# Optimization experiments

Hardware: AMD Instinct MI355X
Metric: run time of the kernel (lower is better)

## Reference

```python
import jax, jax.numpy as jnp
import numpy as np
from jax import lax

BLOCK = 64      # block_size
OVERLAP = 16
NITER = 64      # Niter init kwarg; loop runs min(1000, Niter)
L = 0.24        # diffusion step size
K = 0.03        # exp(logk), logk = log(0.03)
DEPS = 0.1
FFT_STEPS = 10
THRESH = 0.1    # uniform-region variance threshold


def _g(x):
    # g(x) = 1 / (1 + |x^2| / K^2)
    return 1.0 / (1.0 + jnp.abs(x * x) / (K * K))


def _avgpool3(x):
    # F.avg_pool2d(x, 3, stride=1, padding=1) with count_include_pad=True (divide by 9)
    s = lax.reduce_window(x, 0.0, lax.add, (1, 1, 3, 3), (1, 1, 1, 1),
                          [(0, 0), (0, 0), (1, 1), (1, 1)])
    return s / 9.0


def _fft_diffuse_block(block, bcv, bch):
    cv_mean = bcv.mean()
    ch_mean = bch.mean()
    h, w = block.shape[2], block.shape[3]
    ky = jnp.arange(h, dtype=block.dtype)[:, None] * (2.0 * np.pi / h)      # [h,1]
    kx = jnp.arange(w // 2 + 1, dtype=block.dtype)[None, :] * (2.0 * np.pi / w)  # [1,w//2+1]
    op = (1.0 - 2.0 * L * (cv_mean * (1.0 - jnp.cos(ky)) + ch_mean * (1.0 - jnp.cos(kx)))) ** FFT_STEPS
    return jnp.fft.irfft2(jnp.fft.rfft2(block) * op, s=(h, w))


def _forward(guide, initial):
    # depth shift for stability (torch code branches on initial.min() <= deps)
    shift = jnp.where(initial.min() <= DEPS, DEPS, 0.0).astype(initial.dtype)
    depth = initial + shift

    # diffusion coefficients from guide: cv [B,1,H-1,W], ch [B,1,H,W-1]
    cv = _g(jnp.mean(jnp.abs(guide[:, :, 1:, :] - guide[:, :, :-1, :]), axis=1, keepdims=True))
    ch = _g(jnp.mean(jnp.abs(guide[:, :, :, 1:] - guide[:, :, :, :-1]), axis=1, keepdims=True))

    # identify_uniform_regions (local variance via avg pools); original torch code
    # broadcasts shapes (H-1,W) & (H,W-1) which errors -- we crop to common (H-1,W-1)
    cv_var = _avgpool3(cv ** 2) - _avgpool3(cv) ** 2
    ch_var = _avgpool3(ch ** 2) - _avgpool3(ch) ** 2
    uniform = ((cv_var[:, :, :, :-1] < THRESH) & (ch_var[:, :, :-1, :] < THRESH)).astype(depth.dtype)

    B, C, H, W = depth.shape
    step = BLOCK - OVERLAP
    # sequential per-block FFT diffusion with overlap blending (blocks read
    # depth updated by previous blocks, so order matters)
    for b in range(B):
        for y in range(0, H, step):
            for x in range(0, W, step):
                y_end = min(y + BLOCK, H)
                x_end = min(x + BLOCK, W)
                bh, bw = y_end - y, x_end - x
                block = depth[b:b + 1, :, y:y_end, x:x_end]
                bcv = cv[b:b + 1, :, y:y_end - 1, x:x_end]
                bch = ch[b:b + 1, :, y:y_end, x:x_end - 1]
                bun = uniform[b:b + 1, :, y:y_end, x:x_end]  # clips at edges (H-1,W-1)
                cond = bun.mean() > 0.7
                newb = _fft_diffuse_block(block, bcv, bch)
                if y > 0 or x > 0:
                    blend_y = jnp.ones((bh,), depth.dtype)
                    if y > 0:
                        r = jnp.arange(bh)
                        blend_y = jnp.where(r < min(OVERLAP, bh), r.astype(depth.dtype) / OVERLAP, blend_y)
                    blend_x = jnp.ones((bw,), depth.dtype)
                    if x > 0:
                        r = jnp.arange(bw)
                        blend_x = jnp.where(r < min(OVERLAP, bw), r.astype(depth.dtype) / OVERLAP, blend_x)
                    blend = (blend_y[:, None] * blend_x[None, :])[None, None]
                    cand = block * (1.0 - blend) + newb * blend
                else:
                    cand = newb
                region = jnp.where(cond, cand, block)
                depth = depth.at[b:b + 1, :, y:y_end, x:x_end].set(region)

    # explicit anisotropic diffusion stencil, serial data dependence -> lax.scan
    def diffuse_step(I, _):
        dv = I[:, :, 1:, :] - I[:, :, :-1, :]
        dh = I[:, :, :, 1:] - I[:, :, :, :-1]  # computed before vertical update (as in torch)
        tv = L * cv * dv
        I = I.at[:, :, 1:, :].add(-tv).at[:, :, :-1, :].add(tv)
        th = L * ch * dh
        I = I.at[:, :, :, 1:].add(-th).at[:, :, :, :-1].add(th)
        return I, None

    depth, _ = lax.scan(diffuse_step, depth, None, length=min(1000, NITER))
    y_pred = depth - shift
    return y_pred, cv, ch


def setup_inputs() -> dict:
    key = jax.random.key(0)
    k1, k2 = jax.random.split(key)
    guide = jax.random.uniform(k1, (2, 3, 512, 512), dtype=jnp.float32)
    initial = jax.random.uniform(k2, (2, 1, 512, 512), dtype=jnp.float32)
    return {"guide": guide, "initial": initial}


def reference(guide, initial):
    # returns (y_pred, cv, ch) matching {'y_pred':..., 'cv':..., 'ch':...}
    return _forward(guide, initial)
```

## Files before the change

### kernel.cpp

```cpp
#include <hip/hip_runtime.h>
#include <stdint.h>

#define LDIFF 0.24f

constexpr int H = 512, W = 512, NB = 2;
constexpr int HW = H * W;
constexpr int N_D = NB * HW;
constexpr int CVH = 511, CVW = 512;
constexpr int CHH = 512, CHW = 511;
constexpr int N_CV = NB * CVH * CVW;
constexpr int NBLKS = 11;
constexpr int NBT = NB * 121;

__device__ inline float ldc(const float* p) {
    return __hip_atomic_load(p, __ATOMIC_RELAXED, __HIP_MEMORY_SCOPE_AGENT);
}
__device__ inline void stc(float* p, float v) {
    __hip_atomic_store(p, v, __ATOMIC_RELAXED, __HIP_MEMORY_SCOPE_AGENT);
}
__device__ inline int ldci(const int* p) {
    return __hip_atomic_load(p, __ATOMIC_RELAXED, __HIP_MEMORY_SCOPE_AGENT);
}
__device__ inline void stci(int* p, int v) {
    __hip_atomic_store(p, v, __ATOMIC_RELAXED, __HIP_MEMORY_SCOPE_AGENT);
}

__device__ inline float rot_a(float x) {
    return __int_as_float(__builtin_amdgcn_update_dpp(0, __float_as_int(x), 0x134, 0xf, 0xf, false));
}
__device__ inline float rot_b(float x) {
    return __int_as_float(__builtin_amdgcn_update_dpp(0, __float_as_int(x), 0x13c, 0xf, 0xf, false));
}
__device__ inline float sh_a(float x) {
    return __int_as_float(__builtin_amdgcn_update_dpp(0, __float_as_int(x), 0x130, 0xf, 0xf, true));
}
__device__ inline float sh_b(float x) {
    return __int_as_float(__builtin_amdgcn_update_dpp(0, __float_as_int(x), 0x138, 0xf, 0xf, true));
}

__global__ __launch_bounds__(256) void kall(
    const float* __restrict__ guide, const float* __restrict__ initial,
    float* __restrict__ cv, float* __restrict__ ch,
    float* __restrict__ D, float* __restrict__ T0, float* __restrict__ T1,
    float* __restrict__ ypred, int* __restrict__ sync_)
{
    __shared__ float cvT[73 * 74];
    __shared__ float chT[73 * 74];
    __shared__ float xT[2][4][64];
    __shared__ float xB[2][4][64];
    __shared__ float red[12];
    __shared__ float prmS[3];

    int* wflag = sync_;
    int* dflag = sync_ + 16384;

    const int blk = blockIdx.x;
    const int i = blk / NBLKS, j = blk % NBLKS;
    const int b = blockIdx.y;
    const int tid = threadIdx.x;
    const int lane = tid & 63, wv = tid >> 6;
    const int r0 = wv * 16;
    const int me = b * 121 + blk;

    const int y0 = i * 48, x0 = j * 48;
    const int y1 = min(y0 + 64, 512), x1 = min(x0 + 64, 512);
    const int bh = y1 - y0, bw = x1 - x0;
    const int yb = y0 - 8, xb = x0 - 8;
    const float kinv = 1.0f / (0.03f * 0.03f);

    const float* gb = guide + (size_t)b * 3 * HW;
    for (int p = tid; p < 73 * 73; p += 256) {
        int rr = p / 73, cc2 = p - rr * 73;
        int y = yb + rr, x = xb + cc2;
        float cvv = 0.0f, chv = 0.0f;
        if (y >= 0 && y < 512 && x >= 0 && x < 512) {
            const float* g = gb + y * W + x;
            float g0 = g[0], g1 = g[HW], g2 = g[2 * HW];
            if (y < 511) {
                float d = (fabsf(g[W] - g0) + fabsf(g[HW + W] - g1) + fabsf(g[2 * HW + W] - g2)) * (1.0f / 3.0f);
                cvv = 1.0f / (1.0f + d * d * kinv);
            }
            if (x < 511) {
                float d = (fabsf(g[1] - g0) + fabsf(g[HW + 1] - g1) + fabsf(g[2 * HW + 1] - g2)) * (1.0f / 3.0f);
                chv = 1.0f / (1.0f + d * d * kinv);
            }
        }
        cvT[rr * 74 + cc2] = cvv;
        chT[rr * 74 + cc2] = chv;
    }
    __syncthreads();

    {
        int rcv = min(y0 + 48, CVH) - y0, ccv = min(x0 + 48, CVW) - x0;
        float* cvo = cv + b * CVH * CVW;
        for (int p = tid; p < rcv * ccv; p += 256) {
            int r = p / ccv, c = p - r * ccv;
            cvo[(y0 + r) * CVW + x0 + c] = cvT[(r + 8) * 74 + c + 8];
        }
        int rch = min(y0 + 48, CHH) - y0, cch = min(x0 + 48, CHW) - x0;
        float* cho = ch + b * CHH * CHW;
        for (int p = tid; p < rch * cch; p += 256) {
            int r = p / cch, c = p - r * cch;
            cho[(y0 + r) * CHW + x0 + c] = chT[(r + 8) * 74 + c + 8];
        }
    }

    float scv = 0.f, sch = 0.f, sun = 0.f;
    {
        int n = (bh - 1) * bw;
        for (int p = tid; p < n; p += 256) { int r = p / bw, c = p - r * bw; scv += cvT[(r + 8) * 74 + c + 8]; }
    }
    {
        int cols = bw - 1, n = bh * cols;
        for (int p = tid; p < n; p += 256) { int r = p / cols, c = p - r * cols; sch += chT[(r + 8) * 74 + c + 8]; }
    }
    const int ur = min(y1, 511) - y0, uc = min(x1, 511) - x0;
    {
        int n = ur * uc;
        for (int p = tid; p < n; p += 256) {
            int r = p / uc, c = p - r * uc;
            float s1 = 0.f, s2 = 0.f, t1 = 0.f, t2 = 0.f;
            #pragma unroll
            for (int dy = 0; dy < 3; dy++)
                #pragma unroll
                for (int dx = 0; dx < 3; dx++) {
                    float v = cvT[(r + 7 + dy) * 74 + c + 7 + dx]; s1 += v; s2 += v * v;
                    float w2 = chT[(r + 7 + dy) * 74 + c + 7 + dx]; t1 += w2; t2 += w2 * w2;
                }
            float m = s1 * (1.0f / 9.0f);
            float vcv = s2 * (1.0f / 9.0f) - m * m;
            m = t1 * (1.0f / 9.0f);
            float vch = t2 * (1.0f / 9.0f) - m * m;
            if (vcv < 0.1f && vch < 0.1f) sun += 1.f;
        }
    }
    #pragma unroll
    for (int m = 1; m < 64; m <<= 1) {
        scv += __shfl_xor(scv, m);
        sch += __shfl_xor(sch, m);
        sun += __shfl_xor(sun, m);
    }
    if (lane == 0) { red[wv * 3] = scv; red[wv * 3 + 1] = sch; red[wv * 3 + 2] = sun; }
    __syncthreads();
    if (tid == 0) {
        float a0 = red[0] + red[3] + red[6] + red[9];
        float a1 = red[1] + red[4] + red[7] + red[10];
        float a2 = red[2] + red[5] + red[8] + red[11];
        prmS[0] = a0 / (float)((bh - 1) * bw);
        prmS[1] = a1 / (float)(bh * (bw - 1));
        prmS[2] = (a2 / (float)(ur * uc) > 0.7f) ? 1.0f : 0.0f;
    }
    __syncthreads();

    int prb = __builtin_amdgcn_update_dpp(0, lane, 0x134, 0xf, 0xf, false);
    const bool dirL = (prb == ((lane + 63) & 63));

    const bool cond = prmS[2] > 0.5f;
    const float a = LDIFF * prmS[0], bc = LDIFF * prmS[1];
    float* Db = D + b * HW;
    const float* ini = initial + b * HW;

    const int mh = bh - 1, mw = bw - 1;
    const int ccw = lane & mw;

    if (!cond) {
        #pragma unroll
        for (int k = 0; k < 16; k++) {
            int r = r0 + k;
            if (r < bh && (i == 0 || r >= 16) && lane < bw && (j == 0 || lane >= 16)) {
                int ad = (y0 + r) * W + x0 + lane;
                stc(&Db[ad], ini[ad]);
            }
        }
        asm volatile("s_waitcnt vmcnt(0)" ::: "memory");
        if (lane == 0) stci(&wflag[me * 64 + wv * 16], 1);
    } else {
        float u[16], orig[16];
        int addr[16]; bool fD[16];
        #pragma unroll
        for (int k = 0; k < 16; k++) {
            int rr = (r0 + k) & mh;
            addr[k] = (y0 + rr) * W + x0 + ccw;
            fD[k] = (i > 0 && rr < 16) || (j > 0 && ccw < 16);
            if (!fD[k]) orig[k] = ini[addr[k]];
        }
        if (wv == 0) {
            bool need = false;
            const int* fp = &wflag[me * 64];
            if (lane < 3) {
                if (j > 0) { need = true; fp = &wflag[(b * 121 + i * NBLKS + j - 1) * 64 + (lane + 1) * 16]; }
            } else if (lane == 3) {
                if (i > 0) { need = true; fp = &wflag[(b * 121 + (i - 1) * NBLKS + j) * 64 + 3 * 16]; }
            } else if (lane == 4) {
                if (i > 0 && j < 10) { need = true; fp = &wflag[(b * 121 + (i - 1) * NBLKS + j + 1) * 64 + 3 * 16]; }
            } else if (lane == 5) {
                if (i > 0 && j > 0) { need = true; fp = &wflag[(b * 121 + (i - 1) * NBLKS + j - 1) * 64 + 3 * 16]; }
            }
            while (true) {
                int v = need ? ldci(fp) : 1;
                if (__ballot(v == 0) == 0) break;
                __builtin_amdgcn_s_sleep(0);
            }
        }
        __syncthreads();
        #pragma unroll
        for (int k = 0; k < 16; k++) if (fD[k]) orig[k] = ldc(&Db[addr[k]]);
        #pragma unroll
        for (int k = 0; k < 16; k++) u[k] = orig[k];

        int bs = 0;
        for (int it = 0; it < 10; it++) {
            xT[bs][wv][lane] = u[0];
            xB[bs][wv][lane] = u[15];
            __syncthreads();
            float ub = xB[bs][(wv + 3) & 3][lane];
            float ut = xT[bs][(wv + 1) & 3][lane];
            float nu[16];
            #pragma unroll
            for (int k = 0; k < 16; k++) {
                float up = (k == 0) ? ub : u[k - 1];
                float dn = (k == 15) ? ut : u[k + 1];
                float hsum = rot_a(u[k]) + rot_b(u[k]);
                nu[k] = u[k] + a * (up + dn - 2.0f * u[k]) + bc * (hsum - 2.0f * u[k]);
            }
            #pragma unroll
            for (int k = 0; k < 16; k++) u[k] = nu[k];
            bs ^= 1;
        }

        #pragma unroll
        for (int k = 0; k < 16; k++) {
            int r = r0 + k;
            if (r < bh && lane < bw) {
                float byw = (y0 > 0 && r < 16) ? (float)r * (1.0f / 16.0f) : 1.0f;
                float bxw = (x0 > 0 && lane < 16) ? (float)lane * (1.0f / 16.0f) : 1.0f;
                float wgt = byw * bxw;
                stc(&Db[(y0 + r) * W + x0 + lane], orig[k] * (1.0f - wgt) + u[k] * wgt);
            }
        }
        asm volatile("s_waitcnt vmcnt(0)" ::: "memory");
        if (lane == 0) stci(&wflag[me * 64 + wv * 16], 1);
    }
    __syncthreads();

    const int cx = xb + lane;
    const int gxc = min(max(cx, 0), 511);
    float cvr[16], chr[16], chl[16];
    int gyA[16];
    #pragma unroll
    for (int k = 0; k < 16; k++) {
        int cy = yb + r0 + k;
        gyA[k] = min(max(cy, 0), 511);
        cvr[k] = cvT[(r0 + k) * 74 + lane];
        chr[k] = chT[(r0 + k) * 74 + lane];
        chl[k] = dirL ? sh_a(chr[k]) : sh_b(chr[k]);
    }
    const float cvm1 = (wv == 0) ? 0.0f : cvT[(r0 - 1) * 74 + lane];

    float* Tb0 = T0 + b * HW;
    float* Tb1 = T1 + b * HW;
    float* ypb = ypred + b * HW;
    const bool cok = (lane >= 8 && lane < 56 && xb + lane < 512);

    for (int t = 1; t <= 8; t++) {
        if (wv == 0) {
            bool need = false;
            const int* fp = &wflag[me * 64];
            int thr = 1;
            if (t == 1) {
                if (lane < 36) {
                    int nb = lane >> 2;
                    int di = nb / 3 - 1, dj = nb % 3 - 1;
                    int ni = i + di, nj = j + dj;
                    if ((di | dj) != 0 && ni >= 0 && ni < NBLKS && nj >= 0 && nj < NBLKS) {
                        need = true;
                        fp = &wflag[(b * 121 + ni * NBLKS + nj) * 64 + (lane & 3) * 16];
                    }
                }
            } else {
                thr = t - 1;
                if (lane < 9) {
                    int di = lane / 3 - 1, dj = lane % 3 - 1;
                    int ni = i + di, nj = j + dj;
                    if ((di | dj) != 0 && ni >= 0 && ni < NBLKS && nj >= 0 && nj < NBLKS) {
                        need = true;
                        fp = &dflag[(b * 121 + ni * NBLKS + nj) * 16];
                    }
                }
            }
            while (true) {
                int v = need ? ldci(fp) : 0x7fffffff;
                if (__ballot(v < thr) == 0) break;
                __builtin_amdgcn_s_sleep(8);
            }
        }
        __syncthreads();
        const float* src = (t == 1) ? Db : (((t - 1) & 1) ? Tb1 : Tb0);
        float u[16];
        #pragma unroll
        for (int k = 0; k < 16; k++) u[k] = ldc(&src[gyA[k] * W + gxc]);

        int bs = 0;
        for (int it = 0; it < 8; it++) {
            xT[bs][wv][lane] = u[0];
            xB[bs][wv][lane] = u[15];
            __syncthreads();
            float ub = (wv > 0) ? xB[bs][wv - 1][lane] : u[0];
            float ut = (wv < 3) ? xT[bs][wv + 1][lane] : u[15];
            float V[16];
            #pragma unroll
            for (int k = 0; k < 16; k++) {
                float up = (k == 0) ? ub : u[k - 1];
                float dn = (k == 15) ? ut : u[k + 1];
                float cup = (k == 0) ? cvm1 : cvr[k - 1];
                V[k] = u[k] + LDIFF * cvr[k] * (dn - u[k]) - LDIFF * cup * (u[k] - up);
            }
            #pragma unroll
            for (int k = 0; k < 16; k++) {
                float rA = rot_a(V[k]);
                float rB = rot_b(V[k]);
                float lf = dirL ? rA : rB;
                float rt = dirL ? rB : rA;
                u[k] = V[k] + LDIFF * chr[k] * (rt - V[k]) - LDIFF * chl[k] * (V[k] - lf);
            }
            bs ^= 1;
        }

        if (t < 8) {
            float* dst = (t & 1) ? Tb1 : Tb0;
            if (cok) {
                #pragma unroll
                for (int k = 0; k < 16; k++) {
                    int r = r0 + k;
                    if (r >= 8 && r < 56) {
                        int y = yb + r;
                        if (y < 512) stc(&dst[y * W + xb + lane], u[k]);
                    }
                }
            }
            asm volatile("s_waitcnt vmcnt(0)" ::: "memory");
            __syncthreads();
            if (tid == 0) stci(&dflag[me * 16], t);
        } else {
            if (cok) {
                #pragma unroll
                for (int k = 0; k < 16; k++) {
                    int r = r0 + k;
                    if (r >= 8 && r < 56) {
                        int y = yb + r;
                        if (y < 512) ypb[y * W + xb + lane] = u[k];
                    }
                }
            }
        }
    }
}

extern "C" void kernel_launch(void* const* d_in, const int* in_sizes, int n_in,
                              void* d_out, int out_size, void* d_ws, size_t ws_size,
                              hipStream_t stream) {
    const float* guide   = (const float*)d_in[0];
    const float* initial = (const float*)d_in[1];
    float* y_pred = (float*)d_out;
    float* cv = y_pred + N_D;
    float* ch = cv + N_CV;

    uint8_t* w = (uint8_t*)d_ws;
    int* sync_ = (int*)w;
    float* D  = (float*)(w + 131072);
    float* T0 = (float*)(w + 131072 + (size_t)N_D * 4);
    float* T1 = (float*)(w + 131072 + (size_t)2 * N_D * 4);

    (void)hipMemsetAsync(sync_, 0, 131072, stream);
    kall<<<dim3(121, NB), 256, 0, stream>>>(guide, initial, cv, ch, D, T0, T1, y_pred, sync_);
}
```

Baseline: 322.8 us.

## Replace wave flags with sentinel-valued data polling and per-block edge buffers

Drops the per-wave write flags. Workspace data is pre-filled with a 0xFF sentinel, and consumers spin directly on the data values until they differ from the NaN pattern. The sequential block stage now publishes its right and bottom overlap strips into a per-block edge buffer, so the next block can read them without waiting on neighbour flags, and only the interior 48x48 is written to D. This removes flag round-trips and the extra barriers, at the cost of a second large memset and polling many addresses per lane. It also relies on computed values never equalling the sentinel bit pattern.

```diff
diff --git a/kernel.cpp b/kernel.cpp
--- a/kernel.cpp
+++ b/kernel.cpp
@@ -38,11 +38,12 @@
     return __int_as_float(__builtin_amdgcn_update_dpp(0, __float_as_int(x), 0x138, 0xf, 0xf, true));
 }
 
-__global__ __launch_bounds__(256) void kall(
+__global__ __launch_bounds__(256, 1) void kall(
     const float* __restrict__ guide, const float* __restrict__ initial,
     float* __restrict__ cv, float* __restrict__ ch,
-    float* __restrict__ D, float* __restrict__ T0, float* __restrict__ T1,
-    float* __restrict__ ypred, int* __restrict__ sync_)
+    float* __restrict__ D, float* __restrict__ EDG,
+    float* __restrict__ T0, float* __restrict__ T1,
+    float* __restrict__ ypred, int* __restrict__ dflag)
 {
     __shared__ float cvT[73 * 74];
     __shared__ float chT[73 * 74];
@@ -50,9 +51,6 @@
     __shared__ float xB[2][4][64];
     __shared__ float red[12];
     __shared__ float prmS[3];
-
-    int* wflag = sync_;
-    int* dflag = sync_ + 16384;
 
     const int blk = blockIdx.x;
     const int i = blk / NBLKS, j = blk % NBLKS;
@@ -159,55 +157,46 @@
     const float a = LDIFF * prmS[0], bc = LDIFF * prmS[1];
     float* Db = D + b * HW;
     const float* ini = initial + b * HW;
+    float* RG = EDG + (size_t)me * 2048;
+    float* BG = RG + 1024;
 
     const int mh = bh - 1, mw = bw - 1;
     const int ccw = lane & mw;
 
-    if (!cond) {
-        #pragma unroll
-        for (int k = 0; k < 16; k++) {
-            int r = r0 + k;
-            if (r < bh && (i == 0 || r >= 16) && lane < bw && (j == 0 || lane >= 16)) {
-                int ad = (y0 + r) * W + x0 + lane;
-                stc(&Db[ad], ini[ad]);
-            }
-        }
-        asm volatile("s_waitcnt vmcnt(0)" ::: "memory");
-        if (lane == 0) stci(&wflag[me * 64 + wv * 16], 1);
-    } else {
-        float u[16], orig[16];
-        int addr[16]; bool fD[16];
+    float u[16], orig[16];
+    {
+        const int* sp[16];
+        uint32_t pend = 0;
         #pragma unroll
         for (int k = 0; k < 16; k++) {
             int rr = (r0 + k) & mh;
-            addr[k] = (y0 + rr) * W + x0 + ccw;
-            fD[k] = (i > 0 && rr < 16) || (j > 0 && ccw < 16);
-            if (!fD[k]) orig[k] = ini[addr[k]];
-        }
-        if (wv == 0) {
-            bool need = false;
-            const int* fp = &wflag[me * 64];
-            if (lane < 3) {
-                if (j > 0) { need = true; fp = &wflag[(b * 121 + i * NBLKS + j - 1) * 64 + (lane + 1) * 16]; }
-            } else if (lane == 3) {
-                if (i > 0) { need = true; fp = &wflag[(b * 121 + (i - 1) * NBLKS + j) * 64 + 3 * 16]; }
-            } else if (lane == 4) {
-                if (i > 0 && j < 10) { need = true; fp = &wflag[(b * 121 + (i - 1) * NBLKS + j + 1) * 64 + 3 * 16]; }
-            } else if (lane == 5) {
-                if (i > 0 && j > 0) { need = true; fp = &wflag[(b * 121 + (i - 1) * NBLKS + j - 1) * 64 + 3 * 16]; }
-            }
-            while (true) {
-                int v = need ? ldci(fp) : 1;
-                if (__ballot(v == 0) == 0) break;
-                __builtin_amdgcn_s_sleep(0);
-            }
-        }
-        __syncthreads();
-        #pragma unroll
-        for (int k = 0; k < 16; k++) if (fD[k]) orig[k] = ldc(&Db[addr[k]]);
-        #pragma unroll
-        for (int k = 0; k < 16; k++) u[k] = orig[k];
-
+            const float* p = nullptr;
+            if (j > 0 && ccw < 16)
+                p = EDG + (size_t)(me - 1) * 2048 + rr * 16 + ccw;
+            else if (i > 0 && rr < 16)
+                p = (ccw >= 48) ? (EDG + (size_t)(me - NBLKS + 1) * 2048 + 1024 + rr * 64 + (ccw - 48))
+                                : (EDG + (size_t)(me - NBLKS) * 2048 + 1024 + rr * 64 + ccw);
+            sp[k] = (const int*)p;
+            if (p) pend |= 1u << k;
+            else   orig[k] = ini[(y0 + rr) * W + x0 + ccw];
+        }
+        while (pend) {
+            int vv[16];
+            #pragma unroll
+            for (int k = 0; k < 16; k++) if (pend & (1u << k)) vv[k] = ldci(sp[k]);
+            uint32_t np = 0;
+            #pragma unroll
+            for (int k = 0; k < 16; k++) if (pend & (1u << k)) {
+                if (vv[k] != -1) orig[k] = __int_as_float(vv[k]); else np |= 1u << k;
+            }
+            pend = np;
+            if (pend) __builtin_amdgcn_s_sleep(2);
+        }
+    }
+    #pragma unroll
+    for (int k = 0; k < 16; k++) u[k] = orig[k];
+
+    if (cond) {
         int bs = 0;
         for (int it = 0; it < 10; it++) {
             xT[bs][wv][lane] = u[0];
@@ -227,19 +216,27 @@
             for (int k = 0; k < 16; k++) u[k] = nu[k];
             bs ^= 1;
         }
-
-        #pragma unroll
-        for (int k = 0; k < 16; k++) {
-            int r = r0 + k;
-            if (r < bh && lane < bw) {
+    }
+
+    #pragma unroll
+    for (int k = 0; k < 16; k++) {
+        int r = r0 + k;
+        if (r < bh && lane < bw) {
+            if (cond) {
                 float byw = (y0 > 0 && r < 16) ? (float)r * (1.0f / 16.0f) : 1.0f;
                 float bxw = (x0 > 0 && lane < 16) ? (float)lane * (1.0f / 16.0f) : 1.0f;
                 float wgt = byw * bxw;
-                stc(&Db[(y0 + r) * W + x0 + lane], orig[k] * (1.0f - wgt) + u[k] * wgt);
-            }
-        }
-        asm volatile("s_waitcnt vmcnt(0)" ::: "memory");
-        if (lane == 0) stci(&wflag[me * 64 + wv * 16], 1);
+                u[k] = orig[k] * (1.0f - wgt) + u[k] * wgt;
+            }
+            if (bw == 64 && lane >= 48) stc(RG + r * 16 + (lane - 48), u[k]);
+            if (r >= 48)                stc(BG + (r - 48) * 64 + lane, u[k]);
+        }
+    }
+    #pragma unroll
+    for (int k = 0; k < 16; k++) {
+        int r = r0 + k;
+        if (r < 48 && r < bh && lane < 48 && lane < bw)
+            stc(&Db[(y0 + r) * W + x0 + lane], u[k]);
     }
     __syncthreads();
 
@@ -263,22 +260,28 @@
     const bool cok = (lane >= 8 && lane < 56 && xb + lane < 512);
 
     for (int t = 1; t <= 8; t++) {
-        if (wv == 0) {
-            bool need = false;
-            const int* fp = &wflag[me * 64];
-            int thr = 1;
-            if (t == 1) {
-                if (lane < 36) {
-                    int nb = lane >> 2;
-                    int di = nb / 3 - 1, dj = nb % 3 - 1;
-                    int ni = i + di, nj = j + dj;
-                    if ((di | dj) != 0 && ni >= 0 && ni < NBLKS && nj >= 0 && nj < NBLKS) {
-                        need = true;
-                        fp = &wflag[(b * 121 + ni * NBLKS + nj) * 64 + (lane & 3) * 16];
-                    }
-                }
-            } else {
-                thr = t - 1;
+        const float* src = (t == 1) ? Db : (((t - 1) & 1) ? Tb1 : Tb0);
+        float uc2[16];
+        if (t == 1) {
+            uint32_t pend = 0xFFFFu;
+            while (pend) {
+                int vv[16];
+                #pragma unroll
+                for (int k = 0; k < 16; k++) if (pend & (1u << k))
+                    vv[k] = ldci((const int*)(src + gyA[k] * W + gxc));
+                uint32_t np = 0;
+                #pragma unroll
+                for (int k = 0; k < 16; k++) if (pend & (1u << k)) {
+                    if (vv[k] != -1) uc2[k] = __int_as_float(vv[k]); else np |= 1u << k;
+                }
+                pend = np;
+                if (pend) __builtin_amdgcn_s_sleep(2);
+            }
+        } else {
+            if (wv == 0) {
+                bool need = false;
+                const int* fp = dflag;
+                const int thr = t - 1;
                 if (lane < 9) {
                     int di = lane / 3 - 1, dj = lane % 3 - 1;
                     int ni = i + di, nj = j + dj;
@@ -287,33 +290,31 @@
                         fp = &dflag[(b * 121 + ni * NBLKS + nj) * 16];
                     }
                 }
-            }
-            while (true) {
-                int v = need ? ldci(fp) : 0x7fffffff;
-                if (__ballot(v < thr) == 0) break;
-                __builtin_amdgcn_s_sleep(8);
-            }
-        }
-        __syncthreads();
-        const float* src = (t == 1) ? Db : (((t - 1) & 1) ? Tb1 : Tb0);
-        float u[16];
-        #pragma unroll
-        for (int k = 0; k < 16; k++) u[k] = ldc(&src[gyA[k] * W + gxc]);
+                while (true) {
+                    int v = need ? ldci(fp) : 0x7fffffff;
+                    if (__ballot(v < thr) == 0) break;
+                    __builtin_amdgcn_s_sleep(4);
+                }
+            }
+            __syncthreads();
+            #pragma unroll
+            for (int k = 0; k < 16; k++) uc2[k] = ldc(src + gyA[k] * W + gxc);
+        }
 
         int bs = 0;
         for (int it = 0; it < 8; it++) {
-            xT[bs][wv][lane] = u[0];
-            xB[bs][wv][lane] = u[15];
+            xT[bs][wv][lane] = uc2[0];
+            xB[bs][wv][lane] = uc2[15];
             __syncthreads();
-            float ub = (wv > 0) ? xB[bs][wv - 1][lane] : u[0];
-            float ut = (wv < 3) ? xT[bs][wv + 1][lane] : u[15];
+            float ub = (wv > 0) ? xB[bs][wv - 1][lane] : uc2[0];
+            float ut = (wv < 3) ? xT[bs][wv + 1][lane] : uc2[15];
             float V[16];
             #pragma unroll
             for (int k = 0; k < 16; k++) {
-                float up = (k == 0) ? ub : u[k - 1];
-                float dn = (k == 15) ? ut : u[k + 1];
+                float up = (k == 0) ? ub : uc2[k - 1];
+                float dn = (k == 15) ? ut : uc2[k + 1];
                 float cup = (k == 0) ? cvm1 : cvr[k - 1];
-                V[k] = u[k] + LDIFF * cvr[k] * (dn - u[k]) - LDIFF * cup * (u[k] - up);
+                V[k] = uc2[k] + LDIFF * cvr[k] * (dn - uc2[k]) - LDIFF * cup * (uc2[k] - up);
             }
             #pragma unroll
             for (int k = 0; k < 16; k++) {
@@ -321,7 +322,7 @@
                 float rB = rot_b(V[k]);
                 float lf = dirL ? rA : rB;
                 float rt = dirL ? rB : rA;
-                u[k] = V[k] + LDIFF * chr[k] * (rt - V[k]) - LDIFF * chl[k] * (V[k] - lf);
+                uc2[k] = V[k] + LDIFF * chr[k] * (rt - V[k]) - LDIFF * chl[k] * (V[k] - lf);
             }
             bs ^= 1;
         }
@@ -334,7 +335,7 @@
                     int r = r0 + k;
                     if (r >= 8 && r < 56) {
                         int y = yb + r;
-                        if (y < 512) stc(&dst[y * W + xb + lane], u[k]);
+                        if (y < 512) stc(&dst[y * W + xb + lane], uc2[k]);
                     }
                 }
             }
@@ -348,7 +349,7 @@
                     int r = r0 + k;
                     if (r >= 8 && r < 56) {
                         int y = yb + r;
-                        if (y < 512) ypb[y * W + xb + lane] = u[k];
+                        if (y < 512) ypb[y * W + xb + lane] = uc2[k];
                     }
                 }
             }
@@ -366,11 +367,13 @@
     float* ch = cv + N_CV;
 
     uint8_t* w = (uint8_t*)d_ws;
-    int* sync_ = (int*)w;
-    float* D  = (float*)(w + 131072);
-    float* T0 = (float*)(w + 131072 + (size_t)N_D * 4);
-    float* T1 = (float*)(w + 131072 + (size_t)2 * N_D * 4);
-
-    (void)hipMemsetAsync(sync_, 0, 131072, stream);
-    kall<<<dim3(121, NB), 256, 0, stream>>>(guide, initial, cv, ch, D, T0, T1, y_pred, sync_);
-}
+    int* dflag = (int*)w;
+    float* D   = (float*)(w + 65536);
+    float* EDG = (float*)(w + 65536 + (size_t)N_D * 4);
+    float* T0  = (float*)(w + 65536 + (size_t)N_D * 4 + (size_t)NBT * 8192);
+    float* T1  = T0 + N_D;
+
+    (void)hipMemsetAsync(w, 0, 65536, stream);
+    (void)hipMemsetAsync(w + 65536, 0xFF, (size_t)N_D * 4 + (size_t)NBT * 8192, stream);
+    kall<<<dim3(121, NB), 256, 0, stream>>>(guide, initial, cv, ch, D, EDG, T0, T1, y_pred, dflag);
+}
```

Result: slower. 360.6 us (+11.7%).

## Serialize each block-row's FFT-diffusion pass in one workgroup with LDS strip handoff

Applied to the files above, without the earlier changes.

The sequential per-block diffusion pass is now run by the j==0 workgroup of each block row, which walks the 11 blocks left to right. The right overlap strip is passed to the next block through shared memory, and the bottom strip goes to the row below through a separate global strip buffer. This replaces per-workgroup cross-block spin-waits on four quarter flags with one flag per block, plus a parameter-publish flag. The intent is to cut inter-workgroup synchronisation latency along the serial chain, at the cost of serialising each row's work onto a single workgroup while the others idle.

```diff
diff --git a/kernel.cpp b/kernel.cpp
--- a/kernel.cpp
+++ b/kernel.cpp
@@ -41,7 +41,8 @@
 __global__ __launch_bounds__(256) void kall(
     const float* __restrict__ guide, const float* __restrict__ initial,
     float* __restrict__ cv, float* __restrict__ ch,
-    float* __restrict__ D, float* __restrict__ T0, float* __restrict__ T1,
+    float* __restrict__ D, float* __restrict__ BSTR,
+    float* __restrict__ T0, float* __restrict__ T1,
     float* __restrict__ ypred, int* __restrict__ sync_)
 {
     __shared__ float cvT[73 * 74];
@@ -50,9 +51,13 @@
     __shared__ float xB[2][4][64];
     __shared__ float red[12];
     __shared__ float prmS[3];
+    __shared__ float prm2[3];
+    __shared__ float rstrip[64 * 16];
 
     int* wflag = sync_;
-    int* dflag = sync_ + 16384;
+    int* pflag = sync_ + 256;
+    int* dflag = sync_ + 1024;
+    float* PRM = (float*)(sync_ + 8192);
 
     const int blk = blockIdx.x;
     const int i = blk / NBLKS, j = blk % NBLKS;
@@ -149,99 +154,111 @@
         prmS[0] = a0 / (float)((bh - 1) * bw);
         prmS[1] = a1 / (float)(bh * (bw - 1));
         prmS[2] = (a2 / (float)(ur * uc) > 0.7f) ? 1.0f : 0.0f;
+        stc(&PRM[me * 4 + 0], prmS[0]);
+        stc(&PRM[me * 4 + 1], prmS[1]);
+        stc(&PRM[me * 4 + 2], prmS[2]);
     }
     __syncthreads();
+    asm volatile("s_waitcnt vmcnt(0)" ::: "memory");
+    if (tid == 0) stci(&pflag[me], 1);
 
     int prb = __builtin_amdgcn_update_dpp(0, lane, 0x134, 0xf, 0xf, false);
     const bool dirL = (prb == ((lane + 63) & 63));
 
-    const bool cond = prmS[2] > 0.5f;
-    const float a = LDIFF * prmS[0], bc = LDIFF * prmS[1];
     float* Db = D + b * HW;
     const float* ini = initial + b * HW;
 
-    const int mh = bh - 1, mw = bw - 1;
-    const int ccw = lane & mw;
-
-    if (!cond) {
-        #pragma unroll
-        for (int k = 0; k < 16; k++) {
-            int r = r0 + k;
-            if (r < bh && (i == 0 || r >= 16) && lane < bw && (j == 0 || lane >= 16)) {
-                int ad = (y0 + r) * W + x0 + lane;
-                stc(&Db[ad], ini[ad]);
-            }
-        }
-        asm volatile("s_waitcnt vmcnt(0)" ::: "memory");
-        if (lane == 0) stci(&wflag[me * 64 + wv * 16], 1);
-    } else {
-        float u[16], orig[16];
-        int addr[16]; bool fD[16];
-        #pragma unroll
-        for (int k = 0; k < 16; k++) {
-            int rr = (r0 + k) & mh;
-            addr[k] = (y0 + rr) * W + x0 + ccw;
-            fD[k] = (i > 0 && rr < 16) || (j > 0 && ccw < 16);
-            if (!fD[k]) orig[k] = ini[addr[k]];
-        }
-        if (wv == 0) {
-            bool need = false;
-            const int* fp = &wflag[me * 64];
-            if (lane < 3) {
-                if (j > 0) { need = true; fp = &wflag[(b * 121 + i * NBLKS + j - 1) * 64 + (lane + 1) * 16]; }
-            } else if (lane == 3) {
-                if (i > 0) { need = true; fp = &wflag[(b * 121 + (i - 1) * NBLKS + j) * 64 + 3 * 16]; }
-            } else if (lane == 4) {
-                if (i > 0 && j < 10) { need = true; fp = &wflag[(b * 121 + (i - 1) * NBLKS + j + 1) * 64 + 3 * 16]; }
-            } else if (lane == 5) {
-                if (i > 0 && j > 0) { need = true; fp = &wflag[(b * 121 + (i - 1) * NBLKS + j - 1) * 64 + 3 * 16]; }
-            }
-            while (true) {
-                int v = need ? ldci(fp) : 1;
-                if (__ballot(v == 0) == 0) break;
-                __builtin_amdgcn_s_sleep(0);
-            }
-        }
-        __syncthreads();
-        #pragma unroll
-        for (int k = 0; k < 16; k++) if (fD[k]) orig[k] = ldc(&Db[addr[k]]);
-        #pragma unroll
-        for (int k = 0; k < 16; k++) u[k] = orig[k];
-
-        int bs = 0;
-        for (int it = 0; it < 10; it++) {
-            xT[bs][wv][lane] = u[0];
-            xB[bs][wv][lane] = u[15];
-            __syncthreads();
-            float ub = xB[bs][(wv + 3) & 3][lane];
-            float ut = xT[bs][(wv + 1) & 3][lane];
-            float nu[16];
+    if (j == 0) {
+        const int mh = bh - 1;
+        for (int jb = 0; jb < NBLKS; ++jb) {
+            const int xj = jb * 48;
+            const int bwj = min(xj + 64, 512) - xj;
+            const int mwj = bwj - 1;
+            const int ccw = lane & mwj;
+            const int gme = me + jb;
+            const int meU = gme - NBLKS;
+            if (tid == 0) {
+                if (jb > 0) {
+                    while (ldci(&pflag[gme]) == 0) __builtin_amdgcn_s_sleep(0);
+                    prm2[0] = ldc(&PRM[gme * 4]);
+                    prm2[1] = ldc(&PRM[gme * 4 + 1]);
+                    prm2[2] = ldc(&PRM[gme * 4 + 2]);
+                } else {
+                    prm2[0] = prmS[0]; prm2[1] = prmS[1]; prm2[2] = prmS[2];
+                }
+                if (i > 0) {
+                    while (ldci(&wflag[meU]) == 0) __builtin_amdgcn_s_sleep(0);
+                    if (jb < NBLKS - 1)
+                        while (ldci(&wflag[meU + 1]) == 0) __builtin_amdgcn_s_sleep(0);
+                }
+            }
+            __syncthreads();
+            const bool condj = prm2[2] > 0.5f;
+            const float aj = LDIFF * prm2[0], bcj = LDIFF * prm2[1];
+
+            float u[16], orig[16];
             #pragma unroll
             for (int k = 0; k < 16; k++) {
-                float up = (k == 0) ? ub : u[k - 1];
-                float dn = (k == 15) ? ut : u[k + 1];
-                float hsum = rot_a(u[k]) + rot_b(u[k]);
-                nu[k] = u[k] + a * (up + dn - 2.0f * u[k]) + bc * (hsum - 2.0f * u[k]);
-            }
-            #pragma unroll
-            for (int k = 0; k < 16; k++) u[k] = nu[k];
-            bs ^= 1;
-        }
-
-        #pragma unroll
-        for (int k = 0; k < 16; k++) {
-            int r = r0 + k;
-            if (r < bh && lane < bw) {
-                float byw = (y0 > 0 && r < 16) ? (float)r * (1.0f / 16.0f) : 1.0f;
-                float bxw = (x0 > 0 && lane < 16) ? (float)lane * (1.0f / 16.0f) : 1.0f;
-                float wgt = byw * bxw;
-                stc(&Db[(y0 + r) * W + x0 + lane], orig[k] * (1.0f - wgt) + u[k] * wgt);
-            }
-        }
-        asm volatile("s_waitcnt vmcnt(0)" ::: "memory");
-        if (lane == 0) stci(&wflag[me * 64 + wv * 16], 1);
-    }
-    __syncthreads();
+                int rr = (r0 + k) & mh;
+                if (jb > 0 && ccw < 16)
+                    orig[k] = rstrip[rr * 16 + ccw];
+                else if (i > 0 && rr < 16)
+                    orig[k] = (ccw >= 48) ? ldc(&BSTR[(size_t)(meU + 1) * 1024 + rr * 64 + (ccw - 48)])
+                                          : ldc(&BSTR[(size_t)meU * 1024 + rr * 64 + ccw]);
+                else
+                    orig[k] = ini[(y0 + rr) * W + xj + ccw];
+                u[k] = orig[k];
+            }
+
+            if (condj) {
+                int bs = 0;
+                for (int it = 0; it < 10; it++) {
+                    xT[bs][wv][lane] = u[0];
+                    xB[bs][wv][lane] = u[15];
+                    __syncthreads();
+                    float ub = xB[bs][(wv + 3) & 3][lane];
+                    float ut = xT[bs][(wv + 1) & 3][lane];
+                    float nu[16];
+                    #pragma unroll
+                    for (int k = 0; k < 16; k++) {
+                        float up = (k == 0) ? ub : u[k - 1];
+                        float dn = (k == 15) ? ut : u[k + 1];
+                        float hsum = rot_a(u[k]) + rot_b(u[k]);
+                        nu[k] = u[k] + aj * (up + dn - 2.0f * u[k]) + bcj * (hsum - 2.0f * u[k]);
+                    }
+                    #pragma unroll
+                    for (int k = 0; k < 16; k++) u[k] = nu[k];
+                    bs ^= 1;
+                }
+                #pragma unroll
+                for (int k = 0; k < 16; k++) {
+                    int r = r0 + k;
+                    if (r < bh && lane < bwj) {
+                        float byw = (y0 > 0 && r < 16) ? (float)r * (1.0f / 16.0f) : 1.0f;
+                        float bxw = (xj > 0 && lane < 16) ? (float)lane * (1.0f / 16.0f) : 1.0f;
+                        float wgt = byw * bxw;
+                        u[k] = orig[k] * (1.0f - wgt) + u[k] * wgt;
+                    }
+                }
+            }
+            __syncthreads();
+
+            #pragma unroll
+            for (int k = 0; k < 16; k++) {
+                int r = r0 + k;
+                if (r < bh && lane < bwj) {
+                    if (jb < NBLKS - 1 && lane >= 48) rstrip[r * 16 + (lane - 48)] = u[k];
+                    if (i < NBLKS - 1 && r >= 48)
+                        stc(&BSTR[(size_t)gme * 1024 + (r - 48) * 64 + lane], u[k]);
+                    if (r < 48 && lane < 48)
+                        stc(&Db[(y0 + r) * W + xj + lane], u[k]);
+                }
+            }
+            asm volatile("s_waitcnt vmcnt(0)" ::: "memory");
+            __syncthreads();
+            if (tid == 0) stci(&wflag[gme], 1);
+        }
+    }
 
     const int cx = xb + lane;
     const int gxc = min(max(cx, 0), 511);
@@ -263,18 +280,18 @@
     const bool cok = (lane >= 8 && lane < 56 && xb + lane < 512);
 
     for (int t = 1; t <= 8; t++) {
+        const float* src = (t == 1) ? Db : (((t - 1) & 1) ? Tb1 : Tb0);
         if (wv == 0) {
             bool need = false;
-            const int* fp = &wflag[me * 64];
+            const int* fp = wflag;
             int thr = 1;
             if (t == 1) {
-                if (lane < 36) {
-                    int nb = lane >> 2;
-                    int di = nb / 3 - 1, dj = nb % 3 - 1;
+                if (lane < 9) {
+                    int di = lane / 3 - 1, dj = lane % 3 - 1;
                     int ni = i + di, nj = j + dj;
-                    if ((di | dj) != 0 && ni >= 0 && ni < NBLKS && nj >= 0 && nj < NBLKS) {
+                    if (ni >= 0 && ni < NBLKS && nj >= 0 && nj < NBLKS) {
                         need = true;
-                        fp = &wflag[(b * 121 + ni * NBLKS + nj) * 64 + (lane & 3) * 16];
+                        fp = &wflag[b * 121 + ni * NBLKS + nj];
                     }
                 }
             } else {
@@ -295,25 +312,24 @@
             }
         }
         __syncthreads();
-        const float* src = (t == 1) ? Db : (((t - 1) & 1) ? Tb1 : Tb0);
-        float u[16];
+        float uq[16];
         #pragma unroll
-        for (int k = 0; k < 16; k++) u[k] = ldc(&src[gyA[k] * W + gxc]);
+        for (int k = 0; k < 16; k++) uq[k] = ldc(&src[gyA[k] * W + gxc]);
 
         int bs = 0;
         for (int it = 0; it < 8; it++) {
-            xT[bs][wv][lane] = u[0];
-            xB[bs][wv][lane] = u[15];
-            __syncthreads();
-            float ub = (wv > 0) ? xB[bs][wv - 1][lane] : u[0];
-            float ut = (wv < 3) ? xT[bs][wv + 1][lane] : u[15];
+            xT[bs][wv][lane] = uq[0];
+            xB[bs][wv][lane] = uq[15];
+            __syncthreads();
+            float ub = (wv > 0) ? xB[bs][wv - 1][lane] : uq[0];
+            float ut = (wv < 3) ? xT[bs][wv + 1][lane] : uq[15];
             float V[16];
             #pragma unroll
             for (int k = 0; k < 16; k++) {
-                float up = (k == 0) ? ub : u[k - 1];
-                float dn = (k == 15) ? ut : u[k + 1];
+                float up = (k == 0) ? ub : uq[k - 1];
+                float dn = (k == 15) ? ut : uq[k + 1];
                 float cup = (k == 0) ? cvm1 : cvr[k - 1];
-                V[k] = u[k] + LDIFF * cvr[k] * (dn - u[k]) - LDIFF * cup * (u[k] - up);
+                V[k] = uq[k] + LDIFF * cvr[k] * (dn - uq[k]) - LDIFF * cup * (uq[k] - up);
             }
             #pragma unroll
             for (int k = 0; k < 16; k++) {
@@ -321,7 +337,7 @@
                 float rB = rot_b(V[k]);
                 float lf = dirL ? rA : rB;
                 float rt = dirL ? rB : rA;
-                u[k] = V[k] + LDIFF * chr[k] * (rt - V[k]) - LDIFF * chl[k] * (V[k] - lf);
+                uq[k] = V[k] + LDIFF * chr[k] * (rt - V[k]) - LDIFF * chl[k] * (V[k] - lf);
             }
             bs ^= 1;
         }
@@ -334,7 +350,7 @@
                     int r = r0 + k;
                     if (r >= 8 && r < 56) {
                         int y = yb + r;
-                        if (y < 512) stc(&dst[y * W + xb + lane], u[k]);
+                        if (y < 512) stc(&dst[y * W + xb + lane], uq[k]);
                     }
                 }
             }
@@ -348,7 +364,7 @@
                     int r = r0 + k;
                     if (r >= 8 && r < 56) {
                         int y = yb + r;
-                        if (y < 512) ypb[y * W + xb + lane] = u[k];
+                        if (y < 512) ypb[y * W + xb + lane] = uq[k];
                     }
                 }
             }
@@ -367,10 +383,11 @@
 
     uint8_t* w = (uint8_t*)d_ws;
     int* sync_ = (int*)w;
-    float* D  = (float*)(w + 131072);
-    float* T0 = (float*)(w + 131072 + (size_t)N_D * 4);
-    float* T1 = (float*)(w + 131072 + (size_t)2 * N_D * 4);
-
-    (void)hipMemsetAsync(sync_, 0, 131072, stream);
-    kall<<<dim3(121, NB), 256, 0, stream>>>(guide, initial, cv, ch, D, T0, T1, y_pred, sync_);
-}
+    float* D    = (float*)(w + 65536);
+    float* BSTR = D + N_D;
+    float* T0   = BSTR + (size_t)NBT * 1024;
+    float* T1   = T0 + N_D;
+
+    (void)hipMemsetAsync(sync_, 0, 65536, stream);
+    kall<<<dim3(121, NB), 256, 0, stream>>>(guide, initial, cv, ch, D, BSTR, T0, T1, y_pred, sync_);
+}
```

Result: slower. 625.5 us (+93.8%).

## Use halo-widened register tiles to cut per-step barriers in stencil loops

Applied to the files above, without the earlier changes.

Each wave now exchanges a multi-row halo (5 rows for the FFT-approximation loop, 4 for the diffusion loop) through shared memory once, then runs several stencil steps locally on a shrinking register window. This replaces one __syncthreads plus halo exchange per iteration with one per group of iterations. The cost is redundant computation on the halo rows and more registers per thread, which could lower occupancy. The wa/wb arrays grow to about 24-26 floats and the coefficient arrays to 24 entries.

```diff
diff --git a/kernel.cpp b/kernel.cpp
--- a/kernel.cpp
+++ b/kernel.cpp
@@ -38,6 +38,24 @@
     return __int_as_float(__builtin_amdgcn_update_dpp(0, __float_as_int(x), 0x138, 0xf, 0xf, true));
 }
 
+#define BSTEP(SRC, DST, LO, HI)                                                   \
+    _Pragma("unroll")                                                             \
+    for (int m = (LO); m <= (HI); m++) {                                          \
+        float hs = rot_a(SRC[m]) + rot_b(SRC[m]);                                 \
+        DST[m] = SRC[m] + a * (SRC[m - 1] + SRC[m + 1] - 2.0f * SRC[m])           \
+                        + bc * (hs - 2.0f * SRC[m]);                              \
+    }
+
+#define CSTEP(SRC, DST, LO, HI)                                                   \
+    _Pragma("unroll")                                                             \
+    for (int m = (LO); m <= (HI); m++) {                                          \
+        float Vm = SRC[m] + LDIFF * cve[m] * (SRC[m + 1] - SRC[m])                \
+                          - LDIFF * cve[m - 1] * (SRC[m] - SRC[m - 1]);           \
+        float rA = rot_a(Vm), rB = rot_b(Vm);                                     \
+        float lf = dirL ? rA : rB, rt = dirL ? rB : rA;                           \
+        DST[m] = Vm + LDIFF * che[m] * (rt - Vm) - LDIFF * chle[m] * (Vm - lf);   \
+    }
+
 __global__ __launch_bounds__(256) void kall(
     const float* __restrict__ guide, const float* __restrict__ initial,
     float* __restrict__ cv, float* __restrict__ ch,
@@ -46,8 +64,8 @@
 {
     __shared__ float cvT[73 * 74];
     __shared__ float chT[73 * 74];
-    __shared__ float xT[2][4][64];
-    __shared__ float xB[2][4][64];
+    __shared__ float xT[2][4][5][64];
+    __shared__ float xB[2][4][5][64];
     __shared__ float red[12];
     __shared__ float prmS[3];
 
@@ -208,24 +226,29 @@
         #pragma unroll
         for (int k = 0; k < 16; k++) u[k] = orig[k];
 
-        int bs = 0;
-        for (int it = 0; it < 10; it++) {
-            xT[bs][wv][lane] = u[0];
-            xB[bs][wv][lane] = u[15];
+        float wa[26], wb[26];
+        #pragma unroll
+        for (int g = 0; g < 2; ++g) {
+            #pragma unroll
+            for (int q = 0; q < 5; q++) {
+                xT[g][wv][q][lane] = u[q];
+                xB[g][wv][q][lane] = u[11 + q];
+            }
             __syncthreads();
-            float ub = xB[bs][(wv + 3) & 3][lane];
-            float ut = xT[bs][(wv + 1) & 3][lane];
-            float nu[16];
-            #pragma unroll
-            for (int k = 0; k < 16; k++) {
-                float up = (k == 0) ? ub : u[k - 1];
-                float dn = (k == 15) ? ut : u[k + 1];
-                float hsum = rot_a(u[k]) + rot_b(u[k]);
-                nu[k] = u[k] + a * (up + dn - 2.0f * u[k]) + bc * (hsum - 2.0f * u[k]);
-            }
-            #pragma unroll
-            for (int k = 0; k < 16; k++) u[k] = nu[k];
-            bs ^= 1;
+            #pragma unroll
+            for (int q = 0; q < 5; q++) {
+                wa[q]      = xB[g][(wv + 3) & 3][q][lane];
+                wa[21 + q] = xT[g][(wv + 1) & 3][q][lane];
+            }
+            #pragma unroll
+            for (int q = 0; q < 16; q++) wa[5 + q] = u[q];
+            BSTEP(wa, wb, 1, 24);
+            BSTEP(wb, wa, 2, 23);
+            BSTEP(wa, wb, 3, 22);
+            BSTEP(wb, wa, 4, 21);
+            BSTEP(wa, wb, 5, 20);
+            #pragma unroll
+            for (int q = 0; q < 16; q++) u[q] = wb[5 + q];
         }
 
         #pragma unroll
@@ -245,17 +268,21 @@
 
     const int cx = xb + lane;
     const int gxc = min(max(cx, 0), 511);
-    float cvr[16], chr[16], chl[16];
     int gyA[16];
     #pragma unroll
     for (int k = 0; k < 16; k++) {
         int cy = yb + r0 + k;
         gyA[k] = min(max(cy, 0), 511);
-        cvr[k] = cvT[(r0 + k) * 74 + lane];
-        chr[k] = chT[(r0 + k) * 74 + lane];
-        chl[k] = dirL ? sh_a(chr[k]) : sh_b(chr[k]);
-    }
-    const float cvm1 = (wv == 0) ? 0.0f : cvT[(r0 - 1) * 74 + lane];
+    }
+    float cve[24], che[24], chle[24];
+    #pragma unroll
+    for (int m = 0; m < 24; m++) {
+        int rr = r0 + m - 4;
+        bool ok = (rr >= 0);
+        cve[m] = ok ? cvT[rr * 74 + lane] : 0.0f;
+        che[m] = ok ? chT[rr * 74 + lane] : 0.0f;
+        chle[m] = dirL ? sh_a(che[m]) : sh_b(che[m]);
+    }
 
     float* Tb0 = T0 + b * HW;
     float* Tb1 = T1 + b * HW;
@@ -300,30 +327,28 @@
         #pragma unroll
         for (int k = 0; k < 16; k++) u[k] = ldc(&src[gyA[k] * W + gxc]);
 
-        int bs = 0;
-        for (int it = 0; it < 8; it++) {
-            xT[bs][wv][lane] = u[0];
-            xB[bs][wv][lane] = u[15];
+        #pragma unroll
+        for (int g = 0; g < 2; ++g) {
+            #pragma unroll
+            for (int q = 0; q < 4; q++) {
+                xT[g][wv][q][lane] = u[q];
+                xB[g][wv][q][lane] = u[12 + q];
+            }
             __syncthreads();
-            float ub = (wv > 0) ? xB[bs][wv - 1][lane] : u[0];
-            float ut = (wv < 3) ? xT[bs][wv + 1][lane] : u[15];
-            float V[16];
-            #pragma unroll
-            for (int k = 0; k < 16; k++) {
-                float up = (k == 0) ? ub : u[k - 1];
-                float dn = (k == 15) ? ut : u[k + 1];
-                float cup = (k == 0) ? cvm1 : cvr[k - 1];
-                V[k] = u[k] + LDIFF * cvr[k] * (dn - u[k]) - LDIFF * cup * (u[k] - up);
-            }
-            #pragma unroll
-            for (int k = 0; k < 16; k++) {
-                float rA = rot_a(V[k]);
-                float rB = rot_b(V[k]);
-                float lf = dirL ? rA : rB;
-                float rt = dirL ? rB : rA;
-                u[k] = V[k] + LDIFF * chr[k] * (rt - V[k]) - LDIFF * chl[k] * (V[k] - lf);
-            }
-            bs ^= 1;
+            float wa[24], wb[24];
+            #pragma unroll
+            for (int q = 0; q < 4; q++) {
+                wa[q]      = (wv > 0) ? xB[g][wv - 1][q][lane] : u[0];
+                wa[20 + q] = (wv < 3) ? xT[g][wv + 1][q][lane] : u[15];
+            }
+            #pragma unroll
+            for (int q = 0; q < 16; q++) wa[4 + q] = u[q];
+            CSTEP(wa, wb, 1, 22);
+            CSTEP(wb, wa, 2, 21);
+            CSTEP(wa, wb, 3, 20);
+            CSTEP(wb, wa, 4, 19);
+            #pragma unroll
+            for (int q = 0; q < 16; q++) u[q] = wa[4 + q];
         }
 
         if (t < 8) {
```

After: 323.0 us. About the same (+0.0%).
